# Kernel tuning notes

Measured on AMD Instinct MI355X. Metric: run time of the kernel, lower is better.

The kernel has to match this reference:

```python
import jax, jax.numpy as jnp
import numpy as np

MAX_Z = 54  # atomic numbers up to iodine (53)
_mv = np.full(MAX_Z, 4.0, np.float32)
for z, v in {6: 4, 7: 3, 8: 2, 16: 6, 9: 1, 17: 1, 35: 1, 53: 1, 15: 5, 1: 1}.items():
    _mv[z] = v
_vdw = np.full(MAX_Z, 1.6, np.float32)  # default_radius = 1.6
for z, r in {1: 1.2, 6: 1.7, 7: 1.55, 8: 1.52, 9: 1.47, 15: 1.8, 16: 1.8, 17: 1.75, 35: 1.85, 53: 1.98}.items():
    _vdw[z] = r
_bl = np.full((MAX_Z, MAX_Z), 1.5, np.float32)  # default_length = 1.5
for (a, b), L in {(6, 6): 1.54, (6, 7): 1.47, (6, 8): 1.43, (6, 16): 1.82, (6, 9): 1.35, (6, 17): 1.77, (6, 1): 1.09, (7, 7): 1.45, (7, 8): 1.40, (7, 1): 1.01, (8, 8): 1.48, (8, 1): 0.96, (16, 16): 2.05, (15, 8): 1.63}.items():
    _bl[a, b] = L
    _bl[b, a] = L  # symmetric == tuple(sorted(...)) lookup
MAX_VAL = jnp.asarray(_mv)
VDW = jnp.asarray(_vdw)
BOND = jnp.asarray(_bl)
BIG = 1e9  # stands in for torch's float('inf') diagonal mask


def _forward(pos, edge_index, atom_types):
    N = pos.shape[0]
    row, col = edge_index[0], edge_index[1]
    # --- valence violations: scatter-add out-degree per atom ---
    bond_counts = jnp.zeros((N,), pos.dtype).at[row].add(1.0)
    violation = jnp.maximum(bond_counts - MAX_VAL[atom_types], 0.0)  # >0 iff counts > max_val
    loss = jnp.sum(violation ** 2)
    # Sequential valence push. Original loops atoms in ascending order and each atom's
    # neighbors in edge-list order; a stable sort of edges by row reproduces exactly that
    # visitation order, so a scan over sorted edges matches the sequential semantics
    # (pos_new[i] updates feed later direction computations).
    order = jnp.argsort(row)  # jnp.argsort is stable
    rs, cs = row[order], col[order]

    def step(p, rc):
        r, c = rc
        v = violation[r]
        d = p[r] - p[c]
        dist = jnp.linalg.norm(d) + 1e-8
        return p.at[r].add(jnp.where(v > 0, d / dist * v * 1e-3, 0.0)), None

    pos_new, _ = jax.lax.scan(step, pos, (rs, cs))
    # --- bond-length correction (gather per edge, scatter back per atom) ---
    bond_vec = pos_new[row] - pos_new[col]                        # [E,3]
    cur_len = jnp.linalg.norm(bond_vec, axis=-1, keepdims=True)   # [E,1]
    tgt_len = BOND[atom_types[row], atom_types[col]][:, None]     # [E,1]
    loss = loss + jnp.mean(jnp.abs(cur_len - tgt_len) ** 2)
    ratio = jnp.clip(tgt_len / (cur_len + 1e-8), 0.98, 1.02)
    adj = (bond_vec * ratio - bond_vec) * 0.01
    pos_new = pos_new + jnp.zeros_like(pos).at[row].add(adj * 0.5).at[col].add(-adj * 0.5)
    # --- steric clash repulsion over all atom pairs (cdist) ---
    sq = jnp.sum(pos_new ** 2, axis=-1)
    d2 = sq[:, None] + sq[None, :] - 2.0 * (pos_new @ pos_new.T)  # [N,N]
    eye = jnp.eye(N, dtype=bool)
    dist = jnp.sqrt(jnp.maximum(jnp.where(eye, 1.0, d2), 1e-20))
    dist = jnp.where(eye, BIG, dist)  # diagonal masked to +inf in the original
    rad = VDW[atom_types]
    min_d = (rad[:, None] + rad[None, :]) * 0.8
    loss = loss + jnp.sum(jax.nn.relu(min_d - dist) ** 2) / 2.0
    # original loops unordered clash pairs i<j updating i and j symmetrically; the full
    # symmetric double sum below is mathematically identical and avoids an [N,N,3] tensor:
    mask = (dist < min_d) & (dist > 1e-8)
    coeff = jnp.where(mask, (min_d - dist) * 0.005 * 0.5 / dist, 0.0)  # [N,N]
    steric = coeff.sum(axis=1)[:, None] * pos_new - coeff @ pos_new    # sum_j c_ij (p_i - p_j)
    return pos_new + steric, loss * 0.1


def setup_inputs() -> dict:
    key = jax.random.key(0)
    k1, k2, k3, k4 = jax.random.split(key, 4)
    N, E = 8192, 32768
    pos = jax.random.normal(k1, (N, 3), jnp.float32) * 6.0  # coords in an ~Angstrom-scale blob
    elements = jnp.array([1, 6, 7, 8, 9, 15, 16, 17], jnp.int32)  # H C N O F P S Cl
    atom_types = elements[jax.random.randint(k2, (N,), 0, 8)]
    edge_index = jnp.stack([jax.random.randint(k3, (E,), 0, N),
                            jax.random.randint(k4, (E,), 0, N)]).astype(jnp.int32)
    return {"pos": pos, "edge_index": edge_index, "atom_types": atom_types}


def reference(pos, edge_index, atom_types):
    return _forward(pos, edge_index, atom_types)
```

## Files before the change

kernel.cpp:

```cpp
#include <hip/hip_runtime.h>
#include <math.h>

#define NA 8192
#define NE 32768
#define NT 256
#define NCH 33
#define CHUNK 128
#define IBLK 512
#define NIB (NA / IBLK)
#define NPAD 4352
#define NSLICE NCH

#define NBIN 256
#define XMIN (-32.0f)
#define BW 0.25f
#define INVBW 4.0f
#define SKIPM 3.50f
#define BSHIFT 13

#define WS_DEG      0
#define WS_BINCNT   (WS_DEG + NA)
#define WS_MEMSET_N (WS_BINCNT + NBIN)
#define WS_LOSS     WS_MEMSET_N
#define WS_DD       (WS_LOSS + 4)
#define WS_BINSTART (WS_DD + 3*NA)
#define WS_IBBIN    (WS_BINSTART + NBIN)
#define WS_BINOF    (WS_IBBIN + NIB)
#define WS_SPD      ((WS_BINOF + NA + 3) & ~3)
#define WS_SORIG    (WS_SPD + 4*(NA+NPAD))
#define WS_PART     ((WS_SORIG + NA + 3) & ~3)

__device__ __forceinline__ float maxval_of(int z) {
    switch (z) {
        case 1: return 1.f; case 6: return 4.f; case 7: return 3.f; case 8: return 2.f;
        case 9: return 1.f; case 15: return 5.f; case 16: return 6.f; case 17: return 1.f;
        case 35: return 1.f; case 53: return 1.f; default: return 4.f;
    }
}
__device__ __forceinline__ float vdw_of(int z) {
    switch (z) {
        case 1: return 1.2f; case 6: return 1.7f; case 7: return 1.55f; case 8: return 1.52f;
        case 9: return 1.47f; case 15: return 1.8f; case 16: return 1.8f; case 17: return 1.75f;
        case 35: return 1.85f; case 53: return 1.98f; default: return 1.6f;
    }
}
__device__ __forceinline__ float bond_of(int a, int b) {
    int lo = a < b ? a : b, hi = a < b ? b : a;
    switch (lo * 64 + hi) {
        case 6*64+6:   return 1.54f;
        case 6*64+7:   return 1.47f;
        case 6*64+8:   return 1.43f;
        case 6*64+16:  return 1.82f;
        case 6*64+9:   return 1.35f;
        case 6*64+17:  return 1.77f;
        case 1*64+6:   return 1.09f;
        case 7*64+7:   return 1.45f;
        case 7*64+8:   return 1.40f;
        case 1*64+7:   return 1.01f;
        case 8*64+8:   return 1.48f;
        case 1*64+8:   return 0.96f;
        case 16*64+16: return 2.05f;
        case 8*64+15:  return 1.63f;
        default:       return 1.5f;
    }
}
__device__ __forceinline__ float viol_of(int d, int z) {
    return fmaxf((float)d - maxval_of(z), 0.f);
}
__device__ __forceinline__ int bin_of_x(float x) {
    int b = (int)floorf((x - XMIN) * INVBW);
    return min(max(b, 0), NBIN - 1);
}

__device__ __forceinline__ float wave_reduce_sum(float x) {
    #pragma unroll
    for (int off = 32; off > 0; off >>= 1) x += __shfl_down(x, off);
    return x;
}

__global__ void k_deg(const int* __restrict__ row, const float* __restrict__ pos,
                      int* __restrict__ deg, int* __restrict__ binCnt,
                      int* __restrict__ binOf, float4* __restrict__ spd,
                      float* __restrict__ zbase ) {
    int e = blockIdx.x * NT + threadIdx.x;
    if (e < 3 * NA + 4) zbase[e] = 0.f;
    if (e < NPAD) spd[NA + e] = make_float4(1e9f, 1e9f, 1e9f, 0.f);
    if (e < NA) {
        int b = bin_of_x(pos[3*e]);
        int rank = atomicAdd(&binCnt[b], 1);
        binOf[e] = b | (rank << 8);
    }
    if (e < NE) atomicAdd(&deg[row[e]], 1);
}

__global__ void k_edge(const int* __restrict__ row, const int* __restrict__ col,
                       const int* __restrict__ types, const int* __restrict__ deg,
                       const float* __restrict__ pos, float* __restrict__ dD,
                       float* __restrict__ lossAcc) {
    int e = blockIdx.x * NT + threadIdx.x;
    float l1 = 0.f, l0 = 0.f;
    if (e < NE) {
        int r = row[e], c = col[e];
        float bx = pos[3*r]   - pos[3*c];
        float by = pos[3*r+1] - pos[3*c+1];
        float bz = pos[3*r+2] - pos[3*c+2];
        float cur = sqrtf(bx*bx + by*by + bz*bz);
        float tgt = bond_of(types[r], types[c]);
        float diff = cur - tgt;
        l1 = diff * diff;
        float ratio = tgt / (cur + 1e-8f);
        ratio = fminf(fmaxf(ratio, 0.98f), 1.02f);
        float s = (ratio - 1.f) * 0.01f * 0.5f;
        float v = viol_of(deg[r], types[r]);
        float sc = (v > 0.f) ? (v * 1e-3f / (cur + 1e-8f)) : 0.f;
        float rs = s + sc;
        atomicAdd(&dD[3*r],   bx * rs);
        atomicAdd(&dD[3*r+1], by * rs);
        atomicAdd(&dD[3*r+2], bz * rs);
        atomicAdd(&dD[3*c],   -bx * s);
        atomicAdd(&dD[3*c+1], -by * s);
        atomicAdd(&dD[3*c+2], -bz * s);
    }
    if (e < NA) {
        float v = viol_of(deg[e], types[e]);
        l0 = v * v;
    }
    float p1 = wave_reduce_sum(l1);
    float p0 = wave_reduce_sum(l0);
    if ((threadIdx.x & 63) == 0) {
        if (p1 != 0.f) atomicAdd(&lossAcc[1], p1);
        if (p0 != 0.f) atomicAdd(&lossAcc[0], p0);
    }
}

__global__ void k_scatter(const float* __restrict__ pos, const float* __restrict__ dD,
                          const int* __restrict__ types, const int* __restrict__ binOf,
                          const int* __restrict__ binCnt, int* __restrict__ binStartG,
                          int* __restrict__ ibBinG,
                          float4* __restrict__ spd, int* __restrict__ sorig) {
    __shared__ int buf[NBIN];
    __shared__ int sStart[NBIN];
    const int t = threadIdx.x;
    buf[t] = binCnt[t];
    __syncthreads();
    int own = buf[t];
    for (int off = 1; off < NBIN; off <<= 1) {
        int v = (t >= off) ? buf[t - off] : 0;
        __syncthreads();
        buf[t] += v;
        __syncthreads();
    }
    sStart[t] = buf[t] - own;
    if (blockIdx.x == 0) binStartG[t] = sStart[t];
    __syncthreads();
    if (blockIdx.x == 0 && t < NIB) {
        int S = t * IBLK;
        int lo = 0, hi = NBIN;
        while (lo < hi) { int mid = (lo + hi) >> 1;
                          if (sStart[mid] <= S) lo = mid + 1; else hi = mid; }
        ibBinG[t] = lo - 1;
    }
    int a = blockIdx.x * NT + t;
    int v = binOf[a];
    int dst = sStart[v & 255] + (v >> 8);
    spd[dst] = make_float4(pos[3*a]   + dD[3*a],
                           pos[3*a+1] + dD[3*a+1],
                           pos[3*a+2] + dD[3*a+2],
                           vdw_of(types[a]) * 0.8f);
    sorig[dst] = a;
}

__device__ __forceinline__ void steric_pair(const float4 p, const float4 q,
                                            float& cs, float& sx, float& sy, float& sz,
                                            float& ll) {
    float dx = p.x - q.x, dy = p.y - q.y, dz = p.z - q.z;
    float d2 = fmaf(dx, dx, fmaf(dy, dy, dz * dz));
    float md = p.w + q.w;
    float rinv = rsqrtf(fmaxf(d2, 1e-12f));
    float dist = d2 * rinv;
    float t1 = md - dist;
    bool ok = (t1 > 0.f) && (d2 > 1e-12f);
    float t1c = ok ? t1 : 0.f;
    ll = fmaf(t1c, t1c, ll);
    float co = t1c * rinv;
    cs += co;
    sx = fmaf(co, q.x, sx);
    sy = fmaf(co, q.y, sy);
    sz = fmaf(co, q.z, sz);
}

__global__ void __launch_bounds__(NT)
k_steric(const float4* __restrict__ spd, const int* __restrict__ binStart,
         const int* __restrict__ ibBin,
         float4* __restrict__ partial, float* __restrict__ lossAcc) {
    __shared__ float4 sm[CHUNK];
    const int t = threadIdx.x;
    const int b = blockIdx.x;
    const int ib = b / NCH;
    const int c  = b % NCH;
    const int i0 = ib * IBLK + t;
    const int i1 = i0 + NT;
    float xlo = spd[ib * IBLK].x;
    float xhi = spd[ib * IBLK + IBLK - 1].x;
    int bs = ibBin[ib] - BSHIFT; bs = bs < 0 ? 0 : bs;
    const int jbase = binStart[bs] + c * CHUNK;
    if (spd[jbase].x > xhi + SKIPM || spd[jbase + CHUNK - 1].x < xlo - SKIPM) {
        float4 z = make_float4(0.f, 0.f, 0.f, 0.f);
        partial[c * NA + i0] = z;
        partial[c * NA + i1] = z;
        return;
    }
    if (t < CHUNK) sm[t] = spd[jbase + t];
    float4 p0 = spd[i0];
    float4 p1 = spd[i1];
    __syncthreads();
    float cs0 = 0.f, sx0 = 0.f, sy0 = 0.f, sz0 = 0.f, ll0 = 0.f;
    float cs1 = 0.f, sx1 = 0.f, sy1 = 0.f, sz1 = 0.f, ll1 = 0.f;
    #pragma unroll 8
    for (int jj = 0; jj < CHUNK; jj++) {
        float4 q = sm[jj];
        steric_pair(p0, q, cs0, sx0, sy0, sz0, ll0);
        steric_pair(p1, q, cs1, sx1, sy1, sz1, ll1);
    }
    partial[c * NA + i0] = make_float4(cs0, sx0, sy0, sz0);
    partial[c * NA + i1] = make_float4(cs1, sx1, sy1, sz1);
    float part = wave_reduce_sum(ll0 + ll1);
    if ((t & 63) == 0 && part != 0.f) atomicAdd(&lossAcc[2], part);
}

__global__ void k_reduce(const float4* __restrict__ spd, const int* __restrict__ sorig,
                         const float4* __restrict__ partial,
                         const float* __restrict__ lossAcc, float* __restrict__ out) {
    int s = blockIdx.x * NT + threadIdx.x;
    float cs = 0.f, sx = 0.f, sy = 0.f, sz = 0.f;
    #pragma unroll 3
    for (int y = 0; y < NSLICE; y++) {
        float4 u = partial[y * NA + s];
        cs += u.x; sx += u.y; sy += u.z; sz += u.w;
    }
    float4 p = spd[s];
    float c = 1.f + cs * 0.0025f;
    int orig = sorig[s];
    out[3*orig]   = p.x * c - sx * 0.0025f;
    out[3*orig+1] = p.y * c - sy * 0.0025f;
    out[3*orig+2] = p.z * c - sz * 0.0025f;
    if (s == 0) {
        float loss = lossAcc[0] + lossAcc[1] * (1.f / NE) + lossAcc[2] * 0.5f;
        out[3*NA] = loss * 0.1f;
    }
}

extern "C" void kernel_launch(void* const* d_in, const int* in_sizes, int n_in,
                              void* d_out, int out_size, void* d_ws, size_t ws_size,
                              hipStream_t stream) {
    (void)in_sizes; (void)n_in; (void)out_size; (void)ws_size;
    const float* pos   = (const float*)d_in[0];
    const int*   eidx  = (const int*)d_in[1];
    const int*   types = (const int*)d_in[2];
    const int* row = eidx;
    const int* col = eidx + NE;

    int*   ws_i = (int*)d_ws;
    float* ws_f = (float*)d_ws;
    int*    deg      = ws_i + WS_DEG;
    int*    binCnt   = ws_i + WS_BINCNT;
    float*  lossAcc  = ws_f + WS_LOSS;
    float*  dD       = ws_f + WS_DD;
    int*    binStart = ws_i + WS_BINSTART;
    int*    ibBin    = ws_i + WS_IBBIN;
    int*    binOf    = ws_i + WS_BINOF;
    float4* spd      = (float4*)(ws_f + WS_SPD);
    int*    sorig    = ws_i + WS_SORIG;
    float4* partial  = (float4*)(ws_f + WS_PART);
    float*  out      = (float*)d_out;

    hipMemsetAsync(d_ws, 0, (size_t)WS_MEMSET_N * 4, stream);
    k_deg    <<<NE/NT, NT, 0, stream>>>(row, pos, deg, binCnt, binOf, spd,
                                        ws_f + WS_LOSS);
    k_edge   <<<NE/NT, NT, 0, stream>>>(row, col, types, deg, pos, dD, lossAcc);
    k_scatter<<<NA/NT, NT, 0, stream>>>(pos, dD, types, binOf, binCnt,
                                        binStart, ibBin, spd, sorig);
    k_steric <<<NIB*NCH, NT, 0, stream>>>(spd, binStart, ibBin, partial, lossAcc);
    k_reduce <<<NA/NT, NT, 0, stream>>>(spd, sorig, partial, lossAcc, out);
}
```

Measured before the change: 129.2 us.

## Fuse final reduction into steric kernel via last-block-done counters

Removes the separate k_reduce launch. Each steric block bumps a per-i-block counter, and the last block to finish for an i-block sums that block's partials and writes its output. A global counter lets the last finishing i-block write the loss scalar. This saves one kernel launch and its dependency gap, at the cost of extra threadfences and atomics plus a serialized reduction tail in the last block of each i-block.

```diff
diff --git a/kernel.cpp b/kernel.cpp
--- a/kernel.cpp
+++ b/kernel.cpp
@@ -20,7 +20,9 @@
 
 #define WS_DEG      0
 #define WS_BINCNT   (WS_DEG + NA)
-#define WS_MEMSET_N (WS_BINCNT + NBIN)
+#define WS_DONE     (WS_BINCNT + NBIN)
+#define WS_GDONE    (WS_DONE + NIB)
+#define WS_MEMSET_N (WS_GDONE + 1)
 #define WS_LOSS     WS_MEMSET_N
 #define WS_DD       (WS_LOSS + 4)
 #define WS_BINSTART (WS_DD + 3*NA)
@@ -191,9 +193,12 @@
 
 __global__ void __launch_bounds__(NT)
 k_steric(const float4* __restrict__ spd, const int* __restrict__ binStart,
-         const int* __restrict__ ibBin,
-         float4* __restrict__ partial, float* __restrict__ lossAcc) {
+         const int* __restrict__ ibBin, const int* __restrict__ sorig,
+         float4* __restrict__ partial, float* __restrict__ lossAcc,
+         int* __restrict__ done, int* __restrict__ gdone,
+         float* __restrict__ out) {
     __shared__ float4 sm[CHUNK];
+    __shared__ int isLast;
     const int t = threadIdx.x;
     const int b = blockIdx.x;
     const int ib = b / NCH;
@@ -204,49 +209,61 @@
     float xhi = spd[ib * IBLK + IBLK - 1].x;
     int bs = ibBin[ib] - BSHIFT; bs = bs < 0 ? 0 : bs;
     const int jbase = binStart[bs] + c * CHUNK;
-    if (spd[jbase].x > xhi + SKIPM || spd[jbase + CHUNK - 1].x < xlo - SKIPM) {
+    bool skip = (spd[jbase].x > xhi + SKIPM) ||
+                (spd[jbase + CHUNK - 1].x < xlo - SKIPM);
+    if (skip) {
         float4 z = make_float4(0.f, 0.f, 0.f, 0.f);
         partial[c * NA + i0] = z;
         partial[c * NA + i1] = z;
-        return;
-    }
-    if (t < CHUNK) sm[t] = spd[jbase + t];
-    float4 p0 = spd[i0];
-    float4 p1 = spd[i1];
+    } else {
+        if (t < CHUNK) sm[t] = spd[jbase + t];
+        float4 p0 = spd[i0];
+        float4 p1 = spd[i1];
+        __syncthreads();
+        float cs0 = 0.f, sx0 = 0.f, sy0 = 0.f, sz0 = 0.f, ll0 = 0.f;
+        float cs1 = 0.f, sx1 = 0.f, sy1 = 0.f, sz1 = 0.f, ll1 = 0.f;
+        #pragma unroll 8
+        for (int jj = 0; jj < CHUNK; jj++) {
+            float4 q = sm[jj];
+            steric_pair(p0, q, cs0, sx0, sy0, sz0, ll0);
+            steric_pair(p1, q, cs1, sx1, sy1, sz1, ll1);
+        }
+        partial[c * NA + i0] = make_float4(cs0, sx0, sy0, sz0);
+        partial[c * NA + i1] = make_float4(cs1, sx1, sy1, sz1);
+        float part = wave_reduce_sum(ll0 + ll1);
+        if ((t & 63) == 0 && part != 0.f) atomicAdd(&lossAcc[2], part);
+    }
+    __threadfence();
+    if (t == 0) {
+        int old = atomicAdd(&done[ib], 1);
+        isLast = (old == NCH - 1) ? 1 : 0;
+    }
     __syncthreads();
-    float cs0 = 0.f, sx0 = 0.f, sy0 = 0.f, sz0 = 0.f, ll0 = 0.f;
-    float cs1 = 0.f, sx1 = 0.f, sy1 = 0.f, sz1 = 0.f, ll1 = 0.f;
-    #pragma unroll 8
-    for (int jj = 0; jj < CHUNK; jj++) {
-        float4 q = sm[jj];
-        steric_pair(p0, q, cs0, sx0, sy0, sz0, ll0);
-        steric_pair(p1, q, cs1, sx1, sy1, sz1, ll1);
-    }
-    partial[c * NA + i0] = make_float4(cs0, sx0, sy0, sz0);
-    partial[c * NA + i1] = make_float4(cs1, sx1, sy1, sz1);
-    float part = wave_reduce_sum(ll0 + ll1);
-    if ((t & 63) == 0 && part != 0.f) atomicAdd(&lossAcc[2], part);
-}
-
-__global__ void k_reduce(const float4* __restrict__ spd, const int* __restrict__ sorig,
-                         const float4* __restrict__ partial,
-                         const float* __restrict__ lossAcc, float* __restrict__ out) {
-    int s = blockIdx.x * NT + threadIdx.x;
-    float cs = 0.f, sx = 0.f, sy = 0.f, sz = 0.f;
-    #pragma unroll 3
-    for (int y = 0; y < NSLICE; y++) {
-        float4 u = partial[y * NA + s];
-        cs += u.x; sx += u.y; sy += u.z; sz += u.w;
-    }
-    float4 p = spd[s];
-    float c = 1.f + cs * 0.0025f;
-    int orig = sorig[s];
-    out[3*orig]   = p.x * c - sx * 0.0025f;
-    out[3*orig+1] = p.y * c - sy * 0.0025f;
-    out[3*orig+2] = p.z * c - sz * 0.0025f;
-    if (s == 0) {
-        float loss = lossAcc[0] + lossAcc[1] * (1.f / NE) + lossAcc[2] * 0.5f;
-        out[3*NA] = loss * 0.1f;
+    if (!isLast) return;
+    #pragma unroll
+    for (int k = 0; k < 2; k++) {
+        int s = ib * IBLK + k * NT + t;
+        float cs = 0.f, sx = 0.f, sy = 0.f, sz = 0.f;
+        #pragma unroll 3
+        for (int y = 0; y < NSLICE; y++) {
+            float4 u = partial[y * NA + s];
+            cs += u.x; sx += u.y; sy += u.z; sz += u.w;
+        }
+        float4 p = spd[s];
+        float cf = 1.f + cs * 0.0025f;
+        int orig = sorig[s];
+        out[3*orig]   = p.x * cf - sx * 0.0025f;
+        out[3*orig+1] = p.y * cf - sy * 0.0025f;
+        out[3*orig+2] = p.z * cf - sz * 0.0025f;
+    }
+    __syncthreads();
+    if (t == 0) {
+        __threadfence();
+        int g = atomicAdd(gdone, 1);
+        if (g == NIB - 1) {
+            float loss = lossAcc[0] + lossAcc[1] * (1.f / NE) + lossAcc[2] * 0.5f;
+            out[3*NA] = loss * 0.1f;
+        }
     }
 }
 
@@ -264,6 +281,8 @@
     float* ws_f = (float*)d_ws;
     int*    deg      = ws_i + WS_DEG;
     int*    binCnt   = ws_i + WS_BINCNT;
+    int*    done     = ws_i + WS_DONE;
+    int*    gdone    = ws_i + WS_GDONE;
     float*  lossAcc  = ws_f + WS_LOSS;
     float*  dD       = ws_f + WS_DD;
     int*    binStart = ws_i + WS_BINSTART;
@@ -280,6 +299,6 @@
     k_edge   <<<NE/NT, NT, 0, stream>>>(row, col, types, deg, pos, dD, lossAcc);
     k_scatter<<<NA/NT, NT, 0, stream>>>(pos, dD, types, binOf, binCnt,
                                         binStart, ibBin, spd, sorig);
-    k_steric <<<NIB*NCH, NT, 0, stream>>>(spd, binStart, ibBin, partial, lossAcc);
-    k_reduce <<<NA/NT, NT, 0, stream>>>(spd, sorig, partial, lossAcc, out);
-}
+    k_steric <<<NIB*NCH, NT, 0, stream>>>(spd, binStart, ibBin, sorig,
+                                          partial, lossAcc, done, gdone, out);
+}
```

Result: slower. 164.0 us (+26.9%).
